# Optimization experiments

Measured on AMD Instinct MI355X. Metric: run time of the kernel, lower is better.

## Reference

```python
import jax, jax.numpy as jnp
import numpy as np

B, N, C, H, K = 2, 4096, 256, 8, 32
D = C // H
EPS = 1e-5


def _ln(x, w, b):
    # LayerNorm over last axis
    m = x.mean(-1, keepdims=True)
    v = x.var(-1, keepdims=True)
    return (x - m) * jax.lax.rsqrt(v + EPS) * w + b


def setup_inputs() -> dict:
    key = jax.random.key(0)
    ks = jax.random.split(key, 16)
    s = 1.0 / np.sqrt(C)
    inp = {
        'xyz_A': jax.random.normal(ks[0], (B, N, 3), jnp.float32),
        'xyz_B': jax.random.normal(ks[1], (B, N, 3), jnp.float32),
        'featA': jax.random.normal(ks[2], (B, C, N), jnp.float32),
        'featB': jax.random.normal(ks[3], (B, C, N), jnp.float32),
        'ln_in_w': jnp.ones((C,), jnp.float32), 'ln_in_b': jnp.zeros((C,), jnp.float32),
        'wq': jax.random.normal(ks[4], (C, C), jnp.float32) * s, 'bq': jnp.zeros((C,), jnp.float32),
        'wk': jax.random.normal(ks[5], (C, C), jnp.float32) * s, 'bk': jnp.zeros((C,), jnp.float32),
        'wv': jax.random.normal(ks[6], (C, C), jnp.float32) * s, 'bv': jnp.zeros((C,), jnp.float32),
        'wqd': jax.random.normal(ks[7], (C, C), jnp.float32) * s, 'bqd': jnp.zeros((C,), jnp.float32),
        'wkd': jax.random.normal(ks[8], (C, C), jnp.float32) * s, 'bkd': jnp.zeros((C,), jnp.float32),
        'ln_sim_w': jnp.ones((C,), jnp.float32), 'ln_sim_b': jnp.zeros((C,), jnp.float32),
        'ln_dis_w': jnp.ones((C,), jnp.float32), 'ln_dis_b': jnp.zeros((C,), jnp.float32),
        'fus_w1': jax.random.normal(ks[9], (2 * C, 3 * C), jnp.float32) * (1.0 / np.sqrt(3 * C)),
        'bn_g': jnp.ones((2 * C,), jnp.float32), 'bn_b': jnp.zeros((2 * C,), jnp.float32),
        'fus_w2': jax.random.normal(ks[10], (C, 2 * C), jnp.float32) * (1.0 / np.sqrt(2 * C)),
        'fus_b2': jnp.zeros((C,), jnp.float32),
    }
    return inp


def reference(xyz_A, xyz_B, featA, featB, ln_in_w, ln_in_b,
              wq, bq, wk, bk, wv, bv, wqd, bqd, wkd, bkd,
              ln_sim_w, ln_sim_b, ln_dis_w, ln_dis_b,
              fus_w1, bn_g, bn_b, fus_w2, fus_b2):
    xA = featA.transpose(0, 2, 1)   # (B,N,C)
    xB = featB.transpose(0, 2, 1)   # (B,N,C)
    xA_n = _ln(xA, ln_in_w, ln_in_b)

    # KNN: nearest K points of xyz_B for each point in xyz_A
    d2 = (jnp.sum(xyz_A * xyz_A, -1)[:, :, None]
          + jnp.sum(xyz_B * xyz_B, -1)[:, None, :]
          - 2.0 * jnp.einsum('bnc,bmc->bnm', xyz_A, xyz_B))  # (B,N,N)
    _, knn_idx = jax.lax.top_k(-d2, K)  # (B,N,K)

    def proj(x, W, b):  # Conv1d k=1 on (B,N,C)
        return jnp.einsum('bnc,oc->bno', x, W) + b

    def heads(x):
        return x.reshape(B, N, H, D)

    q_s = heads(proj(xA_n, wq, bq))
    k_s = heads(proj(xB, wk, bk))
    v = heads(proj(xB, wv, bv))

    gather = jax.vmap(lambda f, i: f[i])  # (N,H,D),(N,K) -> (N,K,H,D)
    kN = gather(k_s, knn_idx)   # (B,N,K,H,D)
    vN = gather(v, knn_idx)     # (B,N,K,H,D)

    # similarity path: scaled dot-product over K neighbors
    sim = jnp.einsum('bnhd,bnkhd->bnhk', q_s, kN) / jnp.sqrt(jnp.float32(D))
    w_sim = jax.nn.softmax(sim, -1)
    ctx_s = jnp.einsum('bnhk,bnkhd->bnhd', w_sim, vN).reshape(B, N, C)
    ctx_s = _ln(ctx_s, ln_sim_w, ln_sim_b)

    # dissimilarity path: L2 distance scores
    q_d = heads(proj(xA_n, wqd, bqd))
    k_d = heads(proj(xB, wkd, bkd))
    kdN = gather(k_d, knn_idx)  # (B,N,K,H,D)
    diff = q_d[:, :, None] - kdN
    dist = jnp.sqrt(jnp.sum(diff * diff, -1)).transpose(0, 1, 3, 2)  # (B,N,H,K)
    w_dis = jax.nn.softmax(dist, -1)
    ctx_d = jnp.einsum('bnhk,bnkhd->bnhd', w_dis, vN).reshape(B, N, C)
    ctx_d = _ln(ctx_d, ln_dis_w, ln_dis_b)

    # fusion MLP (BN in eval mode: running mean 0, var 1)
    fused = jnp.concatenate([xA_n, ctx_s, ctx_d], -1)  # (B,N,3C)
    y = jnp.einsum('bnc,oc->bno', fused, fus_w1)
    y = y * jax.lax.rsqrt(jnp.float32(1.0 + EPS)) * bn_g + bn_b
    y = jax.nn.relu(y)
    y = jnp.einsum('bnc,oc->bno', y, fus_w2) + fus_b2

    out = y + xA  # residual (identity since in_channel == out_channel)
    return out.transpose(0, 2, 1)  # (B,C,N)
```

## Files before the change

kernel.cpp:

```cpp
#include <hip/hip_runtime.h>
#include <hip/hip_bf16.h>
#include <math.h>

#define B_ 2
#define N_ 4096
#define C_ 256
#define H_ 8
#define K_ 32
#define NP_ (B_*N_)
#define CAPW 256

typedef __attribute__((ext_vector_type(8))) short bf16x8;
typedef __attribute__((ext_vector_type(4))) float f32x4;
typedef __attribute__((ext_vector_type(4))) unsigned short ushort4_t;

__device__ __forceinline__ float bf2f(unsigned short v){
    union { unsigned int u; float f; } x; x.u = ((unsigned int)v) << 16; return x.f;
}
__device__ __forceinline__ unsigned short f2bf(float f){
    union { float f; unsigned int u; } x; x.f = f;
    return (unsigned short)((x.u + 0x7FFFu + ((x.u >> 16) & 1u)) >> 16);
}
__device__ __forceinline__ unsigned int mono(float f){
    union { float f; unsigned int u; } x; x.f = f;
    return x.u ^ (0x80000000u | (unsigned int)((int)x.u >> 31));
}
__device__ __forceinline__ void gload_lds16(const unsigned short* g, unsigned short* l){
    __builtin_amdgcn_global_load_lds(
        (const __attribute__((address_space(1))) unsigned int*)g,
        (__attribute__((address_space(3))) unsigned int*)l, 16, 0, 0);
}

__global__ __launch_bounds__(256) void k_pre(
    const float* __restrict__ s0, const float* __restrict__ s1,
    const float* __restrict__ s2, const float* __restrict__ s3,
    const float* __restrict__ s4, const float* __restrict__ s5,
    const float* __restrict__ s6, unsigned short* __restrict__ Wb,
    const float* __restrict__ xyzB, f32x4* __restrict__ PB,
    const float* __restrict__ xyzA, int* __restrict__ order,
    const float* __restrict__ featA, const float* __restrict__ lnw,
    const float* __restrict__ lnb, unsigned short* __restrict__ F,
    const float* __restrict__ featB, unsigned short* __restrict__ XBT)
{
    __shared__ __align__(16) char smem[35200];
    const int bid = blockIdx.x;
    const int tid = threadIdx.x;
    if (bid < 832){
        int i = (bid*256 + tid)*4;
        const float* s; int off;
        if (i < 327680){
            int seg = i >> 16;
            s = (seg==0)?s0:(seg==1)?s1:(seg==2)?s2:(seg==3)?s3:s4;
            off = i & 65535;
        } else if (i < 720896){
            s = s5; off = i - 327680;
        } else {
            s = s6; off = i - 720896;
        }
        f32x4 v = *(const f32x4*)(s + off);
        ushort4_t o;
        #pragma unroll
        for (int e = 0; e < 4; e++) o[e] = f2bf(v[e]);
        *(ushort4_t*)(Wb + i) = o;
    } else if (bid < 864){
        int i = (bid - 832)*256 + tid;
        float x = xyzB[i*3], y = xyzB[i*3+1], z = xyzB[i*3+2];
        f32x4 o;
        o[0] = -2.f*x; o[1] = -2.f*y; o[2] = -2.f*z;
        o[3] = x*x + y*y + z*z;
        PB[i] = o;
    } else if (bid < 866){
        unsigned int* hist = (unsigned int*)smem;
        unsigned int* wsum = (unsigned int*)(smem + 4096);
        const int b = bid - 864;
        const int wv = tid >> 6, lane = tid & 63;
        for (int i = tid; i < 1024; i += 256) hist[i] = 0u;
        __syncthreads();
        unsigned int code[16];
        #pragma unroll
        for (int i = 0; i < 16; i++){
            const int n = tid + i*256;
            const float* pp = xyzA + (size_t)((b<<12) + n)*3;
            int qx = (int)fminf(fmaxf((pp[0] + 5.f)*1.6f, 0.f), 15.f);
            int qy = (int)fminf(fmaxf((pp[1] + 5.f)*0.8f, 0.f), 7.f);
            int qz = (int)fminf(fmaxf((pp[2] + 5.f)*0.8f, 0.f), 7.f);
            unsigned int c = (unsigned int)((qx & 1) | ((qz & 1) << 1) | ((qy & 1) << 2)
                           | (((qx >> 1) & 1) << 3) | (((qz >> 1) & 1) << 4) | (((qy >> 1) & 1) << 5)
                           | (((qx >> 2) & 1) << 6) | (((qz >> 2) & 1) << 7) | (((qy >> 2) & 1) << 8)
                           | (((qx >> 3) & 1) << 9));
            code[i] = c;
            atomicAdd(&hist[c], 1u);
        }
        __syncthreads();
        unsigned int loc[4], t4 = 0;
        #pragma unroll
        for (int j = 0; j < 4; j++){ loc[j] = hist[tid*4 + j]; t4 += loc[j]; }
        unsigned int sc = t4;
        #pragma unroll
        for (int off = 1; off < 64; off <<= 1){
            unsigned int o = __shfl_up(sc, off, 64);
            if (lane >= off) sc += o;
        }
        if (lane == 63) wsum[wv] = sc;
        __syncthreads();
        unsigned int wb = 0;
        #pragma unroll
        for (int j = 0; j < 4; j++) if (j < wv) wb += wsum[j];
        unsigned int base = wb + sc - t4;
        #pragma unroll
        for (int j = 0; j < 4; j++){ hist[tid*4 + j] = base; base += loc[j]; }
        __syncthreads();
        #pragma unroll
        for (int i = 0; i < 16; i++){
            const int n = tid + i*256;
            unsigned int pos = atomicAdd(&hist[code[i]], 1u);
            order[(b<<12) + pos] = (b<<12) | n;
        }
    } else if (bid < 1122){
        float (*tile)[257] = (float(*)[257])smem;
        float (*ps)[32]    = (float(*)[32])(smem + 32896);
        float (*pq)[32]    = (float(*)[32])(smem + 33920);
        float (*st)[32]    = (float(*)[32])(smem + 34944);
        const int nx = tid & 31, cy = tid >> 5;
        const int pbase = (bid - 866) * 32;
        const int b = pbase >> 12, n0 = pbase & 4095;
        const float* sp = featA + (size_t)b*C_*N_ + n0;
        #pragma unroll 4
        for (int it = 0; it < 32; it++){
            int c = cy + it*8;
            tile[nx][c] = sp[(size_t)c*N_ + nx];
        }
        __syncthreads();
        {
            float s = 0.f, q = 0.f;
            #pragma unroll 8
            for (int i = 0; i < 32; i++){
                int cc = cy*32 + ((i + cy) & 31);
                float x = tile[nx][cc];
                s += x; q = fmaf(x, x, q);
            }
            ps[cy][nx] = s; pq[cy][nx] = q;
        }
        __syncthreads();
        if (tid < 32){
            float S = 0.f, Q = 0.f;
            #pragma unroll
            for (int j = 0; j < 8; j++){ S += ps[j][tid]; Q += pq[j][tid]; }
            float m = S*(1.f/256.f);
            float v = Q*(1.f/256.f) - m*m;
            st[0][tid] = m; st[1][tid] = rsqrtf(v + 1e-5f);
        }
        __syncthreads();
        const int p = pbase + nx;
        const float m = st[0][nx], r = st[1][nx];
        #pragma unroll
        for (int j = 0; j < 4; j++){
            bf16x8 ob;
            #pragma unroll
            for (int e = 0; e < 8; e++){
                int c = cy*32 + j*8 + e;
                ob[e] = (short)f2bf((tile[nx][c]-m)*r*lnw[c] + lnb[c]);
            }
            *(bf16x8*)(F + (size_t)p*768 + cy*32 + j*8) = ob;
        }
    } else {
        float (*tile)[65] = (float(*)[65])smem;
        const int idx = bid - 1122;
        const int x = idx & 63, y = (idx >> 6) & 3, z = idx >> 8;
        const int n0 = x*64, c0 = y*64;
        const int tx = tid & 63, ty = tid >> 6;
        const float* sp = featB + (size_t)z*C_*N_;
        #pragma unroll
        for (int i = 0; i < 16; i++){
            int cr = ty + i*4;
            tile[cr][tx] = sp[(size_t)(c0+cr)*N_ + n0 + tx];
        }
        __syncthreads();
        const int c = c0 + tx;
        #pragma unroll
        for (int i = 0; i < 16; i++){
            int nr = ty + i*4;
            int p = (z<<12) + n0 + nr;
            XBT[(size_t)p*256 + c] = f2bf(tile[tx][nr]);
        }
    }
}

__global__ __launch_bounds__(256) void k_knn(const float* __restrict__ xyzA,
        const f32x4* __restrict__ PB, int* __restrict__ knn){
    const int wv = threadIdx.x >> 6, lane = threadIdx.x & 63;
    const int p = blockIdx.x*4 + wv;
    const int b = p >> 12;
    const f32x4* pb = PB + ((size_t)b << 12);
    const float ax = xyzA[(size_t)p*3], ay = xyzA[(size_t)p*3+1], az = xyzA[(size_t)p*3+2];

    unsigned long long mn = ~0ull;
    #pragma unroll 8
    for (int i = 0; i < 64; i++){
        const int m = i*64 + lane;
        f32x4 c = pb[m];
        float d = fmaf(ax, c[0], fmaf(ay, c[1], fmaf(az, c[2], c[3])));
        unsigned long long key = (((unsigned long long)mono(d)) << 12) | (unsigned int)m;
        mn = key < mn ? key : mn;
    }
    unsigned int rk = 0;
    for (int j = 0; j < 64; j++){
        unsigned long long o = __shfl(mn, j, 64);
        rk += (o < mn) ? 1u : 0u;
    }
    unsigned long long sel = (rk == 31u) ? mn : ~0ull;
    #pragma unroll
    for (int off = 32; off; off >>= 1){
        unsigned long long o = __shfl_xor(sel, off, 64);
        sel = o < sel ? o : sel;
    }
    const unsigned long long v = sel;
    const unsigned int vhi = (unsigned int)(v >> 12);
    const unsigned int vlo = (unsigned int)(v & 0xFFFull);

    __shared__ unsigned long long cand[4][CAPW];
    __shared__ unsigned int cnt[4];
    if (lane == 0) cnt[wv] = 0u;
    #pragma unroll 8
    for (int i = 0; i < 64; i++){
        const int m = i*64 + lane;
        f32x4 c = pb[m];
        float d = fmaf(ax, c[0], fmaf(ay, c[1], fmaf(az, c[2], c[3])));
        unsigned int u = mono(d);
        if (u < vhi || (u == vhi && (unsigned int)m <= vlo)){
            unsigned int slot = atomicAdd(&cnt[wv], 1u);
            if (slot < CAPW)
                cand[wv][slot] = (((unsigned long long)u) << 12) | (unsigned int)m;
        }
    }
    const unsigned int C = cnt[wv];
    if (C <= CAPW){
        for (unsigned int i = lane; i < C; i += 64){
            unsigned long long mk = cand[wv][i];
            unsigned int rank = 0;
            for (unsigned int j = 0; j < C; j++) rank += (cand[wv][j] < mk) ? 1u : 0u;
            if (rank < K_) knn[(size_t)p*K_ + rank] = (int)(mk & 0xFFFull);
        }
    } else {
        unsigned long long last = 0ull;
        for (int it = 0; it < K_; it++){
            unsigned long long cm = ~0ull;
            #pragma unroll 4
            for (int i = 0; i < 64; i++){
                const int m = i*64 + lane;
                f32x4 c = pb[m];
                float d = fmaf(ax, c[0], fmaf(ay, c[1], fmaf(az, c[2], c[3])));
                unsigned long long key = (((unsigned long long)mono(d)) << 12) | (unsigned int)m;
                if (key > last && key < cm) cm = key;
            }
            #pragma unroll
            for (int off = 32; off; off >>= 1){
                unsigned long long o = __shfl_xor(cm, off, 64);
                cm = o < cm ? o : cm;
            }
            if (lane == 0) knn[(size_t)p*K_ + it] = (int)(cm & 0xFFFull);
            last = cm;
        }
    }
}

template<int MODE>
__device__ __forceinline__ void gemm_body(
    const unsigned short* __restrict__ X, int ldx,
    const unsigned short* __restrict__ W, int Kin,
    const float* __restrict__ e0, const float* __restrict__ e1, const float* __restrict__ e2,
    unsigned short* __restrict__ Y, int ldy,
    const float* __restrict__ resid, float* __restrict__ out,
    unsigned short (*As)[128*32], unsigned short (*Bs)[64*32], int bx, int by)
{
    const int tid = threadIdx.x, wid = tid >> 6, lane = tid & 63;
    const int lr = lane & 15, lg = lane >> 4;
    const int m0 = bx*128, n0 = by*64;
    const int lrow = lane >> 2, lcol = (lane & 3)*8;

    const unsigned short* Ag0 = X + (size_t)(m0 + wid*32 + lrow)*ldx + lcol;
    const unsigned short* Ag1 = X + (size_t)(m0 + wid*32 + 16 + lrow)*ldx + lcol;
    const unsigned short* Bg0 = W + (size_t)(n0 + wid*16 + lrow)*Kin + lcol;

    f32x4 acc[2][4] = {};
    const int NT = Kin >> 5;
    int buf = 0;
    gload_lds16(Ag0, &As[0][(wid*32)*32]);
    gload_lds16(Ag1, &As[0][(wid*32+16)*32]);
    gload_lds16(Bg0, &Bs[0][(wid*16)*32]);
    __syncthreads();
    for (int kt = 0; kt < NT; kt++){
        if (kt + 1 < NT){
            const int k = (kt+1)*32;
            gload_lds16(Ag0 + k, &As[buf^1][(wid*32)*32]);
            gload_lds16(Ag1 + k, &As[buf^1][(wid*32+16)*32]);
            gload_lds16(Bg0 + k, &Bs[buf^1][(wid*16)*32]);
        }
        bf16x8 a[2], b[4];
        #pragma unroll
        for (int mi = 0; mi < 2; mi++)
            a[mi] = *(const bf16x8*)&As[buf][(wid*32 + mi*16 + lr)*32 + lg*8];
        #pragma unroll
        for (int ni = 0; ni < 4; ni++)
            b[ni] = *(const bf16x8*)&Bs[buf][(ni*16 + lr)*32 + lg*8];
        #pragma unroll
        for (int mi = 0; mi < 2; mi++){
            #pragma unroll
            for (int ni = 0; ni < 4; ni++)
                acc[mi][ni] = __builtin_amdgcn_mfma_f32_16x16x32_bf16(a[mi], b[ni], acc[mi][ni], 0, 0, 0);
        }
        __syncthreads();
        buf ^= 1;
    }
    #pragma unroll
    for (int mi = 0; mi < 2; mi++){
        const int pbase = m0 + wid*32 + mi*16 + lg*4;
        #pragma unroll
        for (int ni = 0; ni < 4; ni++){
            const int o = n0 + ni*16 + lr;
            if (MODE == 0){
                const float* bp = (o < 256) ? e0 : ((o < 512) ? e1 : e2);
                float bias = bp[o & 255];
                #pragma unroll
                for (int r = 0; r < 4; r++)
                    Y[(size_t)(pbase + r)*ldy + o] = f2bf(acc[mi][ni][r] + bias);
            } else if (MODE == 1){
                float sc = e0[o] * 0.9999950000374997f;
                float sh = e1[o];
                #pragma unroll
                for (int r = 0; r < 4; r++){
                    float vv = fmaf(acc[mi][ni][r], sc, sh);
                    Y[(size_t)(pbase + r)*ldy + o] = f2bf(fmaxf(vv, 0.f));
                }
            } else {
                float bias = e0[o];
                const int b = pbase >> 12, nn = pbase & 4095;
                const size_t adr = ((size_t)b*C_ + o)*N_ + nn;
                f32x4 rv = *(const f32x4*)(resid + adr);
                f32x4 ov;
                #pragma unroll
                for (int r = 0; r < 4; r++) ov[r] = acc[mi][ni][r] + bias + rv[r];
                *(f32x4*)(out + adr) = ov;
            }
        }
    }
}

__global__ __launch_bounds__(256) void k_proj(
    const unsigned short* __restrict__ F, const unsigned short* __restrict__ XBT,
    const unsigned short* __restrict__ WQcat, const unsigned short* __restrict__ WKVD,
    const float* __restrict__ bq, const float* __restrict__ bqd,
    const float* __restrict__ bk, const float* __restrict__ bv, const float* __restrict__ bkd,
    unsigned short* __restrict__ QQ, unsigned short* __restrict__ KVD)
{
    __shared__ __align__(16) unsigned short As[2][128*32];
    __shared__ __align__(16) unsigned short Bs[2][64*32];
    if (blockIdx.y < 8)
        gemm_body<0>(F, 768, WQcat, 256, bq, bqd, nullptr, QQ, 512, nullptr, nullptr,
                     As, Bs, blockIdx.x, blockIdx.y);
    else
        gemm_body<0>(XBT, 256, WKVD, 256, bk, bv, bkd, KVD, 768, nullptr, nullptr,
                     As, Bs, blockIdx.x, blockIdx.y - 8);
}

template<int MODE>
__global__ __launch_bounds__(256) void k_gemm(
    const unsigned short* __restrict__ X, int ldx,
    const unsigned short* __restrict__ W, int Kin,
    const float* __restrict__ e0, const float* __restrict__ e1, const float* __restrict__ e2,
    unsigned short* __restrict__ Y, int ldy,
    const float* __restrict__ resid, float* __restrict__ out)
{
    __shared__ __align__(16) unsigned short As[2][128*32];
    __shared__ __align__(16) unsigned short Bs[2][64*32];
    gemm_body<MODE>(X, ldx, W, Kin, e0, e1, e2, Y, ldy, resid, out,
                    As, Bs, blockIdx.x, blockIdx.y);
}

__global__ __launch_bounds__(128) void k_attn(
    const unsigned short* __restrict__ QQ, const unsigned short* __restrict__ KVD,
    const int* __restrict__ KNN, const int* __restrict__ order,
    const float* __restrict__ lnsw, const float* __restrict__ lnsb,
    const float* __restrict__ lndw, const float* __restrict__ lndb,
    unsigned short* __restrict__ F)
{
    __shared__ float q_l[2][2][128];
    __shared__ float w_l[2][2][4][33];
    __shared__ int   idx_l[2][32];
    __shared__ float part_l[2][4];

    const int tid = threadIdx.x;
    const int wh = tid >> 6, lane = tid & 63;
    const int bid = blockIdx.x;
    const int xcd = bid & 7, ib = bid >> 3;
    const int batch = xcd & 1, quarter = xcd >> 1;
    const int jj = quarter*1024 + ib;
    const int p = order[(batch << 12) + jj];
    const int b = batch;

    {
        const unsigned short* qrow = QQ + (size_t)p*512 + wh*128 + lane*2;
        unsigned int us = *(const unsigned int*)qrow;
        unsigned int ud = *(const unsigned int*)(qrow + 256);
        q_l[wh][0][lane*2]   = bf2f((unsigned short)(us & 0xffff));
        q_l[wh][0][lane*2+1] = bf2f((unsigned short)(us >> 16));
        q_l[wh][1][lane*2]   = bf2f((unsigned short)(ud & 0xffff));
        q_l[wh][1][lane*2+1] = bf2f((unsigned short)(ud >> 16));
        if (lane < 32) idx_l[wh][lane] = KNN[(size_t)p*K_ + lane];
    }

    const int hh = lane >> 5, kk = lane & 31;
    const int tq = lane >> 4, c = lane & 15;
    const int hl = c >> 2;

    const int nbr_qk = idx_l[wh][kk];
    int nbt[8];
    #pragma unroll
    for (int i = 0; i < 8; i++) nbt[i] = idx_l[wh][tq + i*4];

    const unsigned short* rowb = KVD + (size_t)((b<<12) + nbr_qk)*768;
    bf16x8 kx[2][4], dx[2][4];
    #pragma unroll
    for (int j = 0; j < 2; j++){
        const int h = wh*4 + j*2 + hh;
        const bf16x8* kr = (const bf16x8*)(rowb + h*32);
        const bf16x8* dr = (const bf16x8*)(rowb + 512 + h*32);
        #pragma unroll
        for (int cc = 0; cc < 4; cc++){ kx[j][cc] = kr[cc]; dx[j][cc] = dr[cc]; }
    }
    const unsigned short* vbase = KVD + 256 + wh*128 + c*8;
    bf16x8 vx[8];
    #pragma unroll
    for (int i = 0; i < 8; i++)
        vx[i] = *(const bf16x8*)(vbase + (size_t)((b<<12) + nbt[i])*768);

    #pragma unroll
    for (int j = 0; j < 2; j++){
        const int hloc = j*2 + hh;
        const float* qs = &q_l[wh][0][hloc*32];
        const float* qd = &q_l[wh][1][hloc*32];
        float s = 0.f, dd = 0.f;
        #pragma unroll
        for (int cc = 0; cc < 4; cc++){
            #pragma unroll
            for (int e = 0; e < 8; e++){
                const int d = cc*8 + e;
                s = fmaf(qs[d], bf2f((unsigned short)kx[j][cc][e]), s);
                float df = qd[d] - bf2f((unsigned short)dx[j][cc][e]);
                dd = fmaf(df, df, dd);
            }
        }
        float sim = s * 0.17677669529663687f;
        float dist = sqrtf(dd);
        float m1 = sim, m2 = dist;
        #pragma unroll
        for (int off = 1; off < 32; off <<= 1){
            m1 = fmaxf(m1, __shfl_xor(m1, off, 64));
            m2 = fmaxf(m2, __shfl_xor(m2, off, 64));
        }
        float e1v = __expf(sim - m1);
        float e2v = __expf(dist - m2);
        float s1 = e1v, s2 = e2v;
        #pragma unroll
        for (int off = 1; off < 32; off <<= 1){
            s1 += __shfl_xor(s1, off, 64);
            s2 += __shfl_xor(s2, off, 64);
        }
        w_l[wh][0][hloc][kk] = e1v / s1;
        w_l[wh][1][hloc][kk] = e2v / s2;
    }

    float cs[8] = {0,0,0,0,0,0,0,0}, cd[8] = {0,0,0,0,0,0,0,0};
    #pragma unroll
    for (int i = 0; i < 8; i++){
        const int t = tq + i*4;
        const float wsv = w_l[wh][0][hl][t];
        const float wdv = w_l[wh][1][hl][t];
        #pragma unroll
        for (int e = 0; e < 8; e++){
            float vf = bf2f((unsigned short)vx[i][e]);
            cs[e] = fmaf(wsv, vf, cs[e]);
            cd[e] = fmaf(wdv, vf, cd[e]);
        }
    }
    #pragma unroll
    for (int e = 0; e < 8; e++){
        cs[e] += __shfl_xor(cs[e], 16, 64); cs[e] += __shfl_xor(cs[e], 32, 64);
        cd[e] += __shfl_xor(cd[e], 16, 64); cd[e] += __shfl_xor(cd[e], 32, 64);
    }
    float s1 = 0.f, q1 = 0.f, s2 = 0.f, q2 = 0.f;
    #pragma unroll
    for (int e = 0; e < 8; e++){
        s1 += cs[e]; q1 = fmaf(cs[e], cs[e], q1);
        s2 += cd[e]; q2 = fmaf(cd[e], cd[e], q2);
    }
    #pragma unroll
    for (int off = 1; off < 16; off <<= 1){
        s1 += __shfl_xor(s1, off, 64); q1 += __shfl_xor(q1, off, 64);
        s2 += __shfl_xor(s2, off, 64); q2 += __shfl_xor(q2, off, 64);
    }
    if (lane == 0){
        part_l[wh][0] = s1; part_l[wh][1] = q1;
        part_l[wh][2] = s2; part_l[wh][3] = q2;
    }
    __syncthreads();
    const float S1 = s1 + part_l[wh^1][0];
    const float Q1 = q1 + part_l[wh^1][1];
    const float S2 = s2 + part_l[wh^1][2];
    const float Q2 = q2 + part_l[wh^1][3];
    const float m1 = S1*(1.f/256.f), m2 = S2*(1.f/256.f);
    const float r1 = rsqrtf(Q1*(1.f/256.f) - m1*m1 + 1e-5f);
    const float r2 = rsqrtf(Q2*(1.f/256.f) - m2*m2 + 1e-5f);

    if (tq == 0){
        bf16x8 ob;
        #pragma unroll
        for (int e = 0; e < 8; e++){
            const int cg = wh*128 + c*8 + e;
            ob[e] = (short)f2bf((cs[e]-m1)*r1*lnsw[cg] + lnsb[cg]);
        }
        *(bf16x8*)(F + (size_t)p*768 + 256 + wh*128 + c*8) = ob;
    } else if (tq == 1){
        bf16x8 ob;
        #pragma unroll
        for (int e = 0; e < 8; e++){
            const int cg = wh*128 + c*8 + e;
            ob[e] = (short)f2bf((cd[e]-m2)*r2*lndw[cg] + lndb[cg]);
        }
        *(bf16x8*)(F + (size_t)p*768 + 512 + wh*128 + c*8) = ob;
    }
}

extern "C" void kernel_launch(void* const* d_in, const int* in_sizes, int n_in,
                              void* d_out, int out_size, void* d_ws, size_t ws_size,
                              hipStream_t stream)
{
    const float* xyzA   = (const float*)d_in[0];
    const float* xyzB   = (const float*)d_in[1];
    const float* featA  = (const float*)d_in[2];
    const float* featB  = (const float*)d_in[3];
    const float* ln_in_w= (const float*)d_in[4];
    const float* ln_in_b= (const float*)d_in[5];
    const float* wq  = (const float*)d_in[6];
    const float* bq  = (const float*)d_in[7];
    const float* wk  = (const float*)d_in[8];
    const float* bk  = (const float*)d_in[9];
    const float* wv  = (const float*)d_in[10];
    const float* bv  = (const float*)d_in[11];
    const float* wqd = (const float*)d_in[12];
    const float* bqd = (const float*)d_in[13];
    const float* wkd = (const float*)d_in[14];
    const float* bkd = (const float*)d_in[15];
    const float* lnsw = (const float*)d_in[16];
    const float* lnsb = (const float*)d_in[17];
    const float* lndw = (const float*)d_in[18];
    const float* lndb = (const float*)d_in[19];
    const float* fw1 = (const float*)d_in[20];
    const float* bng = (const float*)d_in[21];
    const float* bnb = (const float*)d_in[22];
    const float* fw2 = (const float*)d_in[23];
    const float* fb2 = (const float*)d_in[24];
    float* out = (float*)d_out;
    char* ws = (char*)d_ws;

    unsigned short* F    = (unsigned short*)(ws + 0);
    unsigned short* XBT  = (unsigned short*)(ws + 12582912);
    unsigned short* QQ   = (unsigned short*)(ws + 16777216);
    unsigned short* KVD  = (unsigned short*)(ws + 25165824);
    unsigned short* Y1   = (unsigned short*)(ws + 37748736);
    f32x4*          PB   = (f32x4*)(ws + 37748736);
    int*            KNNi = (int*)(ws + 46137344);
    int*            ORD  = (int*)(ws + 47185920);
    unsigned short* Wb   = (unsigned short*)(ws + 47251456);
    unsigned short* WQcat = Wb;
    unsigned short* WKVD  = Wb + 131072;
    unsigned short* W1b   = Wb + 327680;
    unsigned short* W2b   = Wb + 720896;

    k_pre<<<1634, 256, 0, stream>>>(wq, wqd, wk, wv, wkd, fw1, fw2, Wb,
                                    xyzB, PB, xyzA, ORD,
                                    featA, ln_in_w, ln_in_b, F, featB, XBT);
    k_knn<<<2048, 256, 0, stream>>>(xyzA, PB, KNNi);

    k_proj<<<dim3(64,20), 256, 0, stream>>>(F, XBT, WQcat, WKVD, bq, bqd, bk, bv, bkd, QQ, KVD);

    k_attn<<<8192, 128, 0, stream>>>(QQ, KVD, KNNi, ORD, lnsw, lnsb, lndw, lndb, F);

    k_gemm<1><<<dim3(64,8), 256, 0, stream>>>(F,  768, W1b, 768, bng, bnb, nullptr, Y1, 512, nullptr, nullptr);
    k_gemm<2><<<dim3(64,4), 256, 0, stream>>>(Y1, 512, W2b, 512, fb2, nullptr, nullptr, nullptr, 0, featA, out);
}
```

Before: 139.9 us.

## Remap attention lanes to (neighbor, channel) layout and drop LDS staging

Changes the k_attn work mapping so each lane handles 8 channels of 8 neighbors for K, D and V, instead of one neighbor's full head dimension for the score step. Query values stay in registers and partial dot products are reduced with short shuffles. Softmax weights remain in registers rather than passing through shared memory. This removes the q_l/w_l LDS round trips and the 32-wide shuffle reductions. The cost is more register pressure and different load coalescing for the gathered K/D rows.

```diff
diff --git a/kernel.cpp b/kernel.cpp
--- a/kernel.cpp
+++ b/kernel.cpp
@@ -384,8 +384,6 @@
     const float* __restrict__ lndw, const float* __restrict__ lndb,
     unsigned short* __restrict__ F)
 {
-    __shared__ float q_l[2][2][128];
-    __shared__ float w_l[2][2][4][33];
     __shared__ int   idx_l[2][32];
     __shared__ float part_l[2][4];
 
@@ -394,93 +392,102 @@
     const int bid = blockIdx.x;
     const int xcd = bid & 7, ib = bid >> 3;
     const int batch = xcd & 1, quarter = xcd >> 1;
-    const int jj = quarter*1024 + ib;
-    const int p = order[(batch << 12) + jj];
+    const int p = order[(batch << 12) + quarter*1024 + ib];
     const int b = batch;
 
+    if (lane < 32) idx_l[wh][lane] = KNN[(size_t)p*K_ + lane];
+
+    const int tq = lane >> 4, c = lane & 15;
+
+    float qsf[8], qdf[8];
     {
-        const unsigned short* qrow = QQ + (size_t)p*512 + wh*128 + lane*2;
-        unsigned int us = *(const unsigned int*)qrow;
-        unsigned int ud = *(const unsigned int*)(qrow + 256);
-        q_l[wh][0][lane*2]   = bf2f((unsigned short)(us & 0xffff));
-        q_l[wh][0][lane*2+1] = bf2f((unsigned short)(us >> 16));
-        q_l[wh][1][lane*2]   = bf2f((unsigned short)(ud & 0xffff));
-        q_l[wh][1][lane*2+1] = bf2f((unsigned short)(ud >> 16));
-        if (lane < 32) idx_l[wh][lane] = KNN[(size_t)p*K_ + lane];
-    }
-
-    const int hh = lane >> 5, kk = lane & 31;
-    const int tq = lane >> 4, c = lane & 15;
-    const int hl = c >> 2;
-
-    const int nbr_qk = idx_l[wh][kk];
+        const unsigned short* qrow = QQ + (size_t)p*512 + wh*128 + c*8;
+        bf16x8 qs8 = *(const bf16x8*)(qrow);
+        bf16x8 qd8 = *(const bf16x8*)(qrow + 256);
+        #pragma unroll
+        for (int e = 0; e < 8; e++){
+            qsf[e] = bf2f((unsigned short)qs8[e]);
+            qdf[e] = bf2f((unsigned short)qd8[e]);
+        }
+    }
+    const unsigned short* KB = KVD + (size_t)(b << 12)*768;
     int nbt[8];
     #pragma unroll
     for (int i = 0; i < 8; i++) nbt[i] = idx_l[wh][tq + i*4];
 
-    const unsigned short* rowb = KVD + (size_t)((b<<12) + nbr_qk)*768;
-    bf16x8 kx[2][4], dx[2][4];
-    #pragma unroll
-    for (int j = 0; j < 2; j++){
-        const int h = wh*4 + j*2 + hh;
-        const bf16x8* kr = (const bf16x8*)(rowb + h*32);
-        const bf16x8* dr = (const bf16x8*)(rowb + 512 + h*32);
-        #pragma unroll
-        for (int cc = 0; cc < 4; cc++){ kx[j][cc] = kr[cc]; dx[j][cc] = dr[cc]; }
-    }
-    const unsigned short* vbase = KVD + 256 + wh*128 + c*8;
-    bf16x8 vx[8];
-    #pragma unroll
-    for (int i = 0; i < 8; i++)
-        vx[i] = *(const bf16x8*)(vbase + (size_t)((b<<12) + nbt[i])*768);
-
-    #pragma unroll
-    for (int j = 0; j < 2; j++){
-        const int hloc = j*2 + hh;
-        const float* qs = &q_l[wh][0][hloc*32];
-        const float* qd = &q_l[wh][1][hloc*32];
-        float s = 0.f, dd = 0.f;
-        #pragma unroll
-        for (int cc = 0; cc < 4; cc++){
+    float s[8];
+    {
+        bf16x8 kx[8];
+        #pragma unroll
+        for (int i = 0; i < 8; i++)
+            kx[i] = *(const bf16x8*)(KB + (size_t)nbt[i]*768 + wh*128 + c*8);
+        #pragma unroll
+        for (int i = 0; i < 8; i++){
+            float a = 0.f;
+            #pragma unroll
+            for (int e = 0; e < 8; e++)
+                a = fmaf(qsf[e], bf2f((unsigned short)kx[i][e]), a);
+            s[i] = a;
+        }
+    }
+    float t[8];
+    {
+        bf16x8 dx[8];
+        #pragma unroll
+        for (int i = 0; i < 8; i++)
+            dx[i] = *(const bf16x8*)(KB + (size_t)nbt[i]*768 + 512 + wh*128 + c*8);
+        #pragma unroll
+        for (int i = 0; i < 8; i++){
+            float a = 0.f;
             #pragma unroll
             for (int e = 0; e < 8; e++){
-                const int d = cc*8 + e;
-                s = fmaf(qs[d], bf2f((unsigned short)kx[j][cc][e]), s);
-                float df = qd[d] - bf2f((unsigned short)dx[j][cc][e]);
-                dd = fmaf(df, df, dd);
+                float df = qdf[e] - bf2f((unsigned short)dx[i][e]);
+                a = fmaf(df, df, a);
             }
-        }
-        float sim = s * 0.17677669529663687f;
-        float dist = sqrtf(dd);
-        float m1 = sim, m2 = dist;
-        #pragma unroll
-        for (int off = 1; off < 32; off <<= 1){
-            m1 = fmaxf(m1, __shfl_xor(m1, off, 64));
-            m2 = fmaxf(m2, __shfl_xor(m2, off, 64));
-        }
-        float e1v = __expf(sim - m1);
-        float e2v = __expf(dist - m2);
-        float s1 = e1v, s2 = e2v;
-        #pragma unroll
-        for (int off = 1; off < 32; off <<= 1){
-            s1 += __shfl_xor(s1, off, 64);
-            s2 += __shfl_xor(s2, off, 64);
-        }
-        w_l[wh][0][hloc][kk] = e1v / s1;
-        w_l[wh][1][hloc][kk] = e2v / s2;
-    }
+            t[i] = a;
+        }
+    }
+    bf16x8 vx[8];
+    #pragma unroll
+    for (int i = 0; i < 8; i++)
+        vx[i] = *(const bf16x8*)(KB + (size_t)nbt[i]*768 + 256 + wh*128 + c*8);
+
+    #pragma unroll
+    for (int i = 0; i < 8; i++){
+        s[i] += __shfl_xor(s[i], 1, 64); s[i] += __shfl_xor(s[i], 2, 64);
+        t[i] += __shfl_xor(t[i], 1, 64); t[i] += __shfl_xor(t[i], 2, 64);
+    }
+    float sim[8], dist[8];
+    #pragma unroll
+    for (int i = 0; i < 8; i++){
+        sim[i]  = s[i] * 0.17677669529663687f;
+        dist[i] = sqrtf(t[i]);
+    }
+    float m1 = sim[0], m2 = dist[0];
+    #pragma unroll
+    for (int i = 1; i < 8; i++){ m1 = fmaxf(m1, sim[i]); m2 = fmaxf(m2, dist[i]); }
+    m1 = fmaxf(m1, __shfl_xor(m1, 16, 64)); m1 = fmaxf(m1, __shfl_xor(m1, 32, 64));
+    m2 = fmaxf(m2, __shfl_xor(m2, 16, 64)); m2 = fmaxf(m2, __shfl_xor(m2, 32, 64));
+    float e1[8], e2[8], s1 = 0.f, s2 = 0.f;
+    #pragma unroll
+    for (int i = 0; i < 8; i++){
+        e1[i] = __expf(sim[i] - m1);  s1 += e1[i];
+        e2[i] = __expf(dist[i] - m2); s2 += e2[i];
+    }
+    s1 += __shfl_xor(s1, 16, 64); s1 += __shfl_xor(s1, 32, 64);
+    s2 += __shfl_xor(s2, 16, 64); s2 += __shfl_xor(s2, 32, 64);
+    const float r1i = 1.f / s1, r2i = 1.f / s2;
 
     float cs[8] = {0,0,0,0,0,0,0,0}, cd[8] = {0,0,0,0,0,0,0,0};
     #pragma unroll
     for (int i = 0; i < 8; i++){
-        const int t = tq + i*4;
-        const float wsv = w_l[wh][0][hl][t];
-        const float wdv = w_l[wh][1][hl][t];
+        const float w1 = e1[i] * r1i;
+        const float w2 = e2[i] * r2i;
         #pragma unroll
         for (int e = 0; e < 8; e++){
             float vf = bf2f((unsigned short)vx[i][e]);
-            cs[e] = fmaf(wsv, vf, cs[e]);
-            cd[e] = fmaf(wdv, vf, cd[e]);
+            cs[e] = fmaf(w1, vf, cs[e]);
+            cd[e] = fmaf(w2, vf, cd[e]);
         }
     }
     #pragma unroll
@@ -488,36 +495,36 @@
         cs[e] += __shfl_xor(cs[e], 16, 64); cs[e] += __shfl_xor(cs[e], 32, 64);
         cd[e] += __shfl_xor(cd[e], 16, 64); cd[e] += __shfl_xor(cd[e], 32, 64);
     }
-    float s1 = 0.f, q1 = 0.f, s2 = 0.f, q2 = 0.f;
+    float s1n = 0.f, q1n = 0.f, s2n = 0.f, q2n = 0.f;
     #pragma unroll
     for (int e = 0; e < 8; e++){
-        s1 += cs[e]; q1 = fmaf(cs[e], cs[e], q1);
-        s2 += cd[e]; q2 = fmaf(cd[e], cd[e], q2);
+        s1n += cs[e]; q1n = fmaf(cs[e], cs[e], q1n);
+        s2n += cd[e]; q2n = fmaf(cd[e], cd[e], q2n);
     }
     #pragma unroll
     for (int off = 1; off < 16; off <<= 1){
-        s1 += __shfl_xor(s1, off, 64); q1 += __shfl_xor(q1, off, 64);
-        s2 += __shfl_xor(s2, off, 64); q2 += __shfl_xor(q2, off, 64);
+        s1n += __shfl_xor(s1n, off, 64); q1n += __shfl_xor(q1n, off, 64);
+        s2n += __shfl_xor(s2n, off, 64); q2n += __shfl_xor(q2n, off, 64);
     }
     if (lane == 0){
-        part_l[wh][0] = s1; part_l[wh][1] = q1;
-        part_l[wh][2] = s2; part_l[wh][3] = q2;
+        part_l[wh][0] = s1n; part_l[wh][1] = q1n;
+        part_l[wh][2] = s2n; part_l[wh][3] = q2n;
     }
     __syncthreads();
-    const float S1 = s1 + part_l[wh^1][0];
-    const float Q1 = q1 + part_l[wh^1][1];
-    const float S2 = s2 + part_l[wh^1][2];
-    const float Q2 = q2 + part_l[wh^1][3];
-    const float m1 = S1*(1.f/256.f), m2 = S2*(1.f/256.f);
-    const float r1 = rsqrtf(Q1*(1.f/256.f) - m1*m1 + 1e-5f);
-    const float r2 = rsqrtf(Q2*(1.f/256.f) - m2*m2 + 1e-5f);
+    const float S1 = s1n + part_l[wh^1][0];
+    const float Q1 = q1n + part_l[wh^1][1];
+    const float S2 = s2n + part_l[wh^1][2];
+    const float Q2 = q2n + part_l[wh^1][3];
+    const float mm1 = S1*(1.f/256.f), mm2 = S2*(1.f/256.f);
+    const float rr1 = rsqrtf(Q1*(1.f/256.f) - mm1*mm1 + 1e-5f);
+    const float rr2 = rsqrtf(Q2*(1.f/256.f) - mm2*mm2 + 1e-5f);
 
     if (tq == 0){
         bf16x8 ob;
         #pragma unroll
         for (int e = 0; e < 8; e++){
             const int cg = wh*128 + c*8 + e;
-            ob[e] = (short)f2bf((cs[e]-m1)*r1*lnsw[cg] + lnsb[cg]);
+            ob[e] = (short)f2bf((cs[e]-mm1)*rr1*lnsw[cg] + lnsb[cg]);
         }
         *(bf16x8*)(F + (size_t)p*768 + 256 + wh*128 + c*8) = ob;
     } else if (tq == 1){
@@ -525,7 +532,7 @@
         #pragma unroll
         for (int e = 0; e < 8; e++){
             const int cg = wh*128 + c*8 + e;
-            ob[e] = (short)f2bf((cd[e]-m2)*r2*lndw[cg] + lndb[cg]);
+            ob[e] = (short)f2bf((cd[e]-mm2)*rr2*lndw[cg] + lndb[cg]);
         }
         *(bf16x8*)(F + (size_t)p*768 + 512 + wh*128 + c*8) = ob;
     }
```

New measurement: 129.1 us. 1.08x faster.
